# Kernel tuning notes

Measured on AMD Instinct MI355X. Metric: run time of the kernel, lower is better.

The kernel has to match this reference:

```python
import jax, jax.numpy as jnp
import numpy as np

B, N, C = 1, 2048, 64


def setup_inputs() -> dict:
    key = jax.random.key(0)
    ks = jax.random.split(key, 7)
    X = jax.random.normal(ks[0], (B, N, 3), jnp.float32)
    embs = jax.random.normal(ks[1], (B, N, C), jnp.float32)
    w0 = jax.random.uniform(ks[2], (N,), jnp.float32)
    s0 = jax.random.uniform(ks[3], (N,), jnp.float32)
    paired_mask = jax.random.uniform(ks[4], (B, N, N), jnp.float32)
    # params: xavier_uniform(gain=0.1) + 1.0  ->  ~1.0 with small spread
    depth_factor = 1.0 + 0.05 * jax.random.normal(ks[5], (2 * C, 1), jnp.float32)
    radius_factor = 1.0 + 0.05 * jax.random.normal(ks[6], (2 * C, 1), jnp.float32)
    return {"X": X, "embs": embs, "w0": w0, "s0": s0, "paired_mask": paired_mask,
            "depth_factor": depth_factor, "radius_factor": radius_factor}


def reference(X, embs, w0, s0, paired_mask, depth_factor, radius_factor):
    c = embs.shape[-1]
    # pairwise distances; torch adds 1e-6 per coordinate before the sum
    V = X[:, None, :, :] - X[:, :, None, :]            # (B,N,N,3), V[b,i,j] = X[b,j]-X[b,i]
    D = jnp.sqrt(jnp.sum(V * V + 1e-6, axis=-1))       # (B,N,N)

    # emb_ij[b,i,j] = concat(embs[b,j], embs[b,i]); matmul with (2C,1) factor
    # splits exactly into two per-node dot products broadcast over the pair grid,
    # so the (B,N,N,2C) concat tensor never needs to be materialized.
    sig_r = jax.nn.sigmoid(embs @ radius_factor[c:, 0][:, None] .squeeze(-1)[:, :, None]
                           + (embs @ radius_factor[:c, 0][:, None]).squeeze(-1)[:, None, :]) if False else \
        jax.nn.sigmoid(jnp.einsum('bnc,c->bn', embs, radius_factor[c:, 0])[:, :, None]
                       + jnp.einsum('bnc,c->bn', embs, radius_factor[:c, 0])[:, None, :])  # (B,N,N)
    sig_d = jax.nn.sigmoid(jnp.einsum('bnc,c->bn', embs, depth_factor[c:, 0])[:, :, None]
                           + jnp.einsum('bnc,c->bn', embs, depth_factor[:c, 0])[:, None, :])  # (B,N,N)

    s0_ij = (s0[None, :] + s0[:, None])[None, None]    # (1,1,N,N)
    s = s0_ij * (0.8 * sig_r + 0.4)                    # (B,B(=1),N,N)

    repl = 5.0 * jnp.exp(-0.3 * D * D * D) * paired_mask   # (B,N,N)

    Dm = D - s                                          # (1,1,N,N) via broadcast
    attr = (jnp.exp(-(Dm - 0.3) * (Dm - 0.3))
            + jnp.exp(-3.0 * Dm * Dm)
            + jnp.exp(-10.0 * Dm * Dm)) / 3.0 * paired_mask

    w0_ij = jnp.sqrt(w0[None, :] * w0[:, None] + 1e-6)[None, None]  # (1,1,N,N)
    w = w0_ij * (sig_d + 0.5)

    Etotal = jnp.sum(-w * attr + repl[None])            # scalar
    Etotal = jnp.where(jnp.isnan(Etotal), jnp.float32(1e-6), Etotal)
    return Etotal
```

## Files before the change

kernel.cpp:

```cpp
#include <hip/hip_runtime.h>

#define NN 2048
#define CC 64

__global__ void prep_kernel(const float* __restrict__ embs,
                            const float* __restrict__ depth_factor,
                            const float* __restrict__ radius_factor,
                            const float* __restrict__ s0,
                            const float* __restrict__ w0,
                            float4* __restrict__ pj,
                            float* __restrict__ ih,
                            float* __restrict__ out) {
    int gid = blockIdx.x * blockDim.x + threadIdx.x;
    if (gid == 0) out[0] = 0.0f;

    int node = gid >> 6;
    int lane = threadIdx.x & 63;
    if (node >= NN) return;

    float e  = embs[node * CC + lane];
    float rl = e * radius_factor[lane];
    float rh = e * radius_factor[CC + lane];
    float dl = e * depth_factor[lane];
    float dh = e * depth_factor[CC + lane];

    #pragma unroll
    for (int off = 32; off > 0; off >>= 1) {
        rl += __shfl_down(rl, off, 64);
        rh += __shfl_down(rh, off, 64);
        dl += __shfl_down(dl, off, 64);
        dh += __shfl_down(dh, off, 64);
    }
    if (lane == 0) {
        pj[node] = make_float4(rl, dl, s0[node], w0[node]);
        ih[node]      = rh;
        ih[NN + node] = dh;
    }
}

__device__ __forceinline__ float pair_e(float xj, float yj, float zj,
                                        float4 p, float m,
                                        float xi, float yi, float zi,
                                        float rhi, float dhi,
                                        float s0i, float w0i) {
    float dx = xj - xi, dy = yj - yi, dz = zj - zi;
    float d2 = fmaf(dx, dx, fmaf(dy, dy, fmaf(dz, dz, 3e-6f)));
    float D  = __builtin_amdgcn_sqrtf(d2);

    float sig_r = __builtin_amdgcn_rcpf(1.0f + __expf(-(rhi + p.x)));
    float sig_d = __builtin_amdgcn_rcpf(1.0f + __expf(-(dhi + p.y)));

    float s  = (s0i + p.z) * fmaf(0.8f, sig_r, 0.4f);
    float Dm = D - s;

    float repl = 5.0f * __expf(-0.3f * d2 * D);

    float e1 = __expf(-Dm * Dm);
    float g  = __expf(fmaf(0.6f, Dm, -0.09f));
    float e2 = e1 * e1;
    float e4 = e2 * e2;
    float e8 = e4 * e4;
    float attr3 = fmaf(e1, g, e2 * e1) + e8 * e2;

    float w = __builtin_amdgcn_sqrtf(fmaf(w0i, p.w, 1e-6f)) * (sig_d + 0.5f);

    return m * fmaf(-w * (1.0f / 3.0f), attr3, repl);
}

__global__ __launch_bounds__(256) void pair_energy_kernel(
        const float* __restrict__ X,
        const float* __restrict__ mask,
        const float4* __restrict__ pj,
        const float* __restrict__ ih,
        float* __restrict__ out) {
    const int i = blockIdx.x;
    const float xi  = X[3 * i];
    const float yi  = X[3 * i + 1];
    const float zi  = X[3 * i + 2];
    const float rhi = ih[i];
    const float dhi = ih[NN + i];
    const float4 pi = pj[i];
    const float s0i = pi.z;
    const float w0i = pi.w;

    const float4* __restrict__ mrow = (const float4*)(mask + (size_t)i * NN);
    const float4* __restrict__ X4   = (const float4*)X;

    float acc = 0.0f;
    #pragma unroll
    for (int it = 0; it < NN / (4 * 256); ++it) {
        int j4 = threadIdx.x + it * 256;
        float4 m  = mrow[j4];
        float4 xa = X4[3 * j4];
        float4 xb = X4[3 * j4 + 1];
        float4 xc = X4[3 * j4 + 2];
        float4 p0 = pj[4 * j4];
        float4 p1 = pj[4 * j4 + 1];
        float4 p2 = pj[4 * j4 + 2];
        float4 p3 = pj[4 * j4 + 3];

        acc += pair_e(xa.x, xa.y, xa.z, p0, m.x, xi, yi, zi, rhi, dhi, s0i, w0i);
        acc += pair_e(xa.w, xb.x, xb.y, p1, m.y, xi, yi, zi, rhi, dhi, s0i, w0i);
        acc += pair_e(xb.z, xb.w, xc.x, p2, m.z, xi, yi, zi, rhi, dhi, s0i, w0i);
        acc += pair_e(xc.y, xc.z, xc.w, p3, m.w, xi, yi, zi, rhi, dhi, s0i, w0i);
    }

    #pragma unroll
    for (int off = 32; off > 0; off >>= 1) acc += __shfl_down(acc, off, 64);

    __shared__ float red[4];
    int lane = threadIdx.x & 63;
    int wid  = threadIdx.x >> 6;
    if (lane == 0) red[wid] = acc;
    __syncthreads();
    if (threadIdx.x == 0) {
        atomicAdd(out, red[0] + red[1] + red[2] + red[3]);
    }
}

extern "C" void kernel_launch(void* const* d_in, const int* in_sizes, int n_in,
                              void* d_out, int out_size, void* d_ws, size_t ws_size,
                              hipStream_t stream) {
    const float* X             = (const float*)d_in[0];
    const float* embs          = (const float*)d_in[1];
    const float* w0            = (const float*)d_in[2];
    const float* s0            = (const float*)d_in[3];
    const float* paired_mask   = (const float*)d_in[4];
    const float* depth_factor  = (const float*)d_in[5];
    const float* radius_factor = (const float*)d_in[6];

    float*  out = (float*)d_out;
    float4* pj  = (float4*)d_ws;
    float*  ih  = (float*)d_ws + 4 * NN;

    prep_kernel<<<dim3(NN / 4), dim3(256), 0, stream>>>(
        embs, depth_factor, radius_factor, s0, w0, pj, ih, out);

    pair_energy_kernel<<<dim3(NN), dim3(256), 0, stream>>>(
        X, paired_mask, pj, ih, out);
}
```

Measured before the change: 105.4 us.

## Factor sigmoid exps and weight sqrt per node; process two rows per block

Precomputes exp(-a) per node, so each pairwise sigmoid becomes rcp(1 + Ei*Ej) with no per-pair exp. The weight term is factored as sqrt(w0i)*sqrt(w0j), dropping the per-pair sqrt and the 1e-6 epsilon. Each block now handles two rows i, reusing the loaded X and per-node j data across both and halving the grid. Risks: the product of exps can overflow for large logits, the epsilon is dropped, and register pressure rises.

```diff
diff --git a/kernel.cpp b/kernel.cpp
--- a/kernel.cpp
+++ b/kernel.cpp
@@ -32,23 +32,24 @@
         dh += __shfl_down(dh, off, 64);
     }
     if (lane == 0) {
-        pj[node] = make_float4(rl, dl, s0[node], w0[node]);
-        ih[node]      = rh;
-        ih[NN + node] = dh;
+        pj[node] = make_float4(__expf(-rl), __expf(-dl),
+                               s0[node], __builtin_amdgcn_sqrtf(w0[node]));
+        ih[node]      = __expf(-rh);
+        ih[NN + node] = __expf(-dh);
     }
 }
 
 __device__ __forceinline__ float pair_e(float xj, float yj, float zj,
                                         float4 p, float m,
                                         float xi, float yi, float zi,
-                                        float rhi, float dhi,
-                                        float s0i, float w0i) {
+                                        float Eri, float Edi,
+                                        float s0i, float swi) {
     float dx = xj - xi, dy = yj - yi, dz = zj - zi;
     float d2 = fmaf(dx, dx, fmaf(dy, dy, fmaf(dz, dz, 3e-6f)));
     float D  = __builtin_amdgcn_sqrtf(d2);
 
-    float sig_r = __builtin_amdgcn_rcpf(1.0f + __expf(-(rhi + p.x)));
-    float sig_d = __builtin_amdgcn_rcpf(1.0f + __expf(-(dhi + p.y)));
+    float sig_r = __builtin_amdgcn_rcpf(fmaf(Eri, p.x, 1.0f));
+    float sig_d = __builtin_amdgcn_rcpf(fmaf(Edi, p.y, 1.0f));
 
     float s  = (s0i + p.z) * fmaf(0.8f, sig_r, 0.4f);
     float Dm = D - s;
@@ -62,7 +63,7 @@
     float e8 = e4 * e4;
     float attr3 = fmaf(e1, g, e2 * e1) + e8 * e2;
 
-    float w = __builtin_amdgcn_sqrtf(fmaf(w0i, p.w, 1e-6f)) * (sig_d + 0.5f);
+    float w = swi * p.w * (sig_d + 0.5f);
 
     return m * fmaf(-w * (1.0f / 3.0f), attr3, repl);
 }
@@ -73,24 +74,25 @@
         const float4* __restrict__ pj,
         const float* __restrict__ ih,
         float* __restrict__ out) {
-    const int i = blockIdx.x;
-    const float xi  = X[3 * i];
-    const float yi  = X[3 * i + 1];
-    const float zi  = X[3 * i + 2];
-    const float rhi = ih[i];
-    const float dhi = ih[NN + i];
-    const float4 pi = pj[i];
-    const float s0i = pi.z;
-    const float w0i = pi.w;
+    const int i0 = 2 * blockIdx.x;
+    const int i1 = i0 + 1;
 
-    const float4* __restrict__ mrow = (const float4*)(mask + (size_t)i * NN);
-    const float4* __restrict__ X4   = (const float4*)X;
+    const float x0 = X[3 * i0], y0 = X[3 * i0 + 1], z0 = X[3 * i0 + 2];
+    const float x1 = X[3 * i1], y1 = X[3 * i1 + 1], z1 = X[3 * i1 + 2];
+    const float Er0 = ih[i0],      Er1 = ih[i1];
+    const float Ed0 = ih[NN + i0], Ed1 = ih[NN + i1];
+    const float4 q0 = pj[i0], q1 = pj[i1];
+
+    const float4* __restrict__ mrow0 = (const float4*)(mask + (size_t)i0 * NN);
+    const float4* __restrict__ mrow1 = (const float4*)(mask + (size_t)i1 * NN);
+    const float4* __restrict__ X4    = (const float4*)X;
 
     float acc = 0.0f;
     #pragma unroll
     for (int it = 0; it < NN / (4 * 256); ++it) {
         int j4 = threadIdx.x + it * 256;
-        float4 m  = mrow[j4];
+        float4 m0 = mrow0[j4];
+        float4 m1 = mrow1[j4];
         float4 xa = X4[3 * j4];
         float4 xb = X4[3 * j4 + 1];
         float4 xc = X4[3 * j4 + 2];
@@ -99,10 +101,15 @@
         float4 p2 = pj[4 * j4 + 2];
         float4 p3 = pj[4 * j4 + 3];
 
-        acc += pair_e(xa.x, xa.y, xa.z, p0, m.x, xi, yi, zi, rhi, dhi, s0i, w0i);
-        acc += pair_e(xa.w, xb.x, xb.y, p1, m.y, xi, yi, zi, rhi, dhi, s0i, w0i);
-        acc += pair_e(xb.z, xb.w, xc.x, p2, m.z, xi, yi, zi, rhi, dhi, s0i, w0i);
-        acc += pair_e(xc.y, xc.z, xc.w, p3, m.w, xi, yi, zi, rhi, dhi, s0i, w0i);
+        acc += pair_e(xa.x, xa.y, xa.z, p0, m0.x, x0, y0, z0, Er0, Ed0, q0.z, q0.w);
+        acc += pair_e(xa.w, xb.x, xb.y, p1, m0.y, x0, y0, z0, Er0, Ed0, q0.z, q0.w);
+        acc += pair_e(xb.z, xb.w, xc.x, p2, m0.z, x0, y0, z0, Er0, Ed0, q0.z, q0.w);
+        acc += pair_e(xc.y, xc.z, xc.w, p3, m0.w, x0, y0, z0, Er0, Ed0, q0.z, q0.w);
+
+        acc += pair_e(xa.x, xa.y, xa.z, p0, m1.x, x1, y1, z1, Er1, Ed1, q1.z, q1.w);
+        acc += pair_e(xa.w, xb.x, xb.y, p1, m1.y, x1, y1, z1, Er1, Ed1, q1.z, q1.w);
+        acc += pair_e(xb.z, xb.w, xc.x, p2, m1.z, x1, y1, z1, Er1, Ed1, q1.z, q1.w);
+        acc += pair_e(xc.y, xc.z, xc.w, p3, m1.w, x1, y1, z1, Er1, Ed1, q1.z, q1.w);
     }
 
     #pragma unroll
@@ -136,6 +143,6 @@
     prep_kernel<<<dim3(NN / 4), dim3(256), 0, stream>>>(
         embs, depth_factor, radius_factor, s0, w0, pj, ih, out);
 
-    pair_energy_kernel<<<dim3(NN), dim3(256), 0, stream>>>(
+    pair_energy_kernel<<<dim3(NN / 2), dim3(256), 0, stream>>>(
         X, paired_mask, pj, ih, out);
 }
```

New measurement: 93.03 us. 1.13x faster.
